# Performance work log

Hardware: AMD Instinct MI355X
Metric: run time of the kernel (lower is better)

The kernel has to match this reference:

```python
import jax, jax.numpy as jnp
import numpy as np

B, S, E = 2, 4096, 512

def setup_inputs() -> dict:
    key = jax.random.key(0)
    kx, kq, kk, kv, ko = jax.random.split(key, 5)
    scale = 1.0 / np.sqrt(E)  # init-style scaling for weights
    return {
        "x": jax.random.normal(kx, (B, S, E), dtype=jnp.float32),
        "Wq": jax.random.normal(kq, (E, E), dtype=jnp.float32) * scale,
        "Wk": jax.random.normal(kk, (E, E), dtype=jnp.float32) * scale,
        "Wv": jax.random.normal(kv, (E, E), dtype=jnp.float32) * scale,
        "Wo": jax.random.normal(ko, (E, E), dtype=jnp.float32) * scale,
        "bo": jnp.zeros((E,), dtype=jnp.float32),
    }

def reference(x, Wq, Wk, Wv, Wo, bo):
    # nn.Linear: y = x @ W.T  (weights stored [out, in])
    q = jnp.einsum("bse,fe->bsf", x, Wq)
    k = jnp.einsum("bse,fe->bsf", x, Wk)
    v = jnp.einsum("bse,fe->bsf", x, Wv)
    inv_scale = 1.0 / jnp.sqrt(jnp.asarray(x.shape[-1], x.dtype))
    scores = jnp.einsum("bqe,bke->bqk", q, k) * inv_scale  # [B,S,S]
    S_len = x.shape[1]
    # torch.triu(ones) keeps j >= i; masked_fill where triu==0 masks j < i
    row = jnp.arange(S_len)[:, None]
    col = jnp.arange(S_len)[None, :]
    keep = col >= row  # [S,S], faithfully anti-causal as in the source
    scores = jnp.where(keep[None, :, :], scores, jnp.asarray(-jnp.inf, scores.dtype))
    attn = jax.nn.softmax(scores, axis=-1)
    # dropout p=0.0 -> identity
    out = jnp.einsum("bqk,bke->bqe", attn, v)
    return jnp.einsum("bse,fe->bsf", out, Wo) + bo
```

## Files before the change

### kernel.cpp

```cpp
#include <hip/hip_runtime.h>
#include <hip/hip_bf16.h>

#define S_LEN 4096
#define E_DIM 512
#define B_DIM 2
#define M_ROWS (B_DIM * S_LEN)

typedef __attribute__((ext_vector_type(8))) short short8;
typedef __attribute__((ext_vector_type(4))) float floatx4;

__device__ __forceinline__ unsigned short f2bf(float f) {
    unsigned u = __float_as_uint(f);
    unsigned r = (u + 0x7fffu + ((u >> 16) & 1u)) >> 16;
    return (unsigned short)r;
}
__device__ __forceinline__ float bf2f(unsigned short u) {
    return __uint_as_float((unsigned)u << 16);
}

__device__ __forceinline__ void async_copy16(unsigned short* lds, const unsigned short* g) {
    auto gp = (const __attribute__((address_space(1))) unsigned int*)g;
    auto lp = (__attribute__((address_space(3))) unsigned int*)lds;
    __builtin_amdgcn_global_load_lds(gp, lp, 16, 0, 0);
}

struct MapArg { unsigned short m[576]; };

__global__ __launch_bounds__(256) void convert_bf16(
    const float* __restrict__ x,  const float* __restrict__ wq,
    const float* __restrict__ wk, const float* __restrict__ wv,
    const float* __restrict__ wo, unsigned short* __restrict__ dstU,
    unsigned short* __restrict__ dstWo)
{
    long i = (long)blockIdx.x * 1024 + (long)threadIdx.x * 4;
    const float* src; long off; unsigned short* dst; long doff;
    if      (i < 4194304) { src = x;  off = i;           dst = dstU;  doff = i; }
    else if (i < 4456448) { src = wq; off = i - 4194304; dst = dstU;  doff = i; }
    else if (i < 4718592) { src = wk; off = i - 4456448; dst = dstU;  doff = i; }
    else if (i < 4980736) { src = wv; off = i - 4718592; dst = dstU;  doff = i; }
    else                  { src = wo; off = i - 4980736; dst = dstWo; doff = i - 4980736; }
    float4 v = *(const float4*)(src + off);
    ushort4 o;
    o.x = f2bf(v.x); o.y = f2bf(v.y); o.z = f2bf(v.z); o.w = f2bf(v.w);
    *(ushort4*)(dst + doff) = o;
}

__device__ __forceinline__ void gemm_core(
    const unsigned short* __restrict__ A, const unsigned short* __restrict__ W,
    void* __restrict__ Cv, const float* __restrict__ bias, int mode,
    int m0, int n0)
{
    __shared__ unsigned short As[128 * 64];
    __shared__ unsigned short Bs[128 * 64];
    const int tid = threadIdx.x;
    const int lane = tid & 63, wave = tid >> 6;
    const int wm = wave >> 1, wn = wave & 1;
    const int q4 = lane >> 4, l16 = lane & 15;
    const int er = l16 & 7;

    floatx4 acc[4][4];
#pragma unroll
    for (int i = 0; i < 4; ++i)
#pragma unroll
        for (int j = 0; j < 4; ++j) acc[i][j] = (floatx4){0.f, 0.f, 0.f, 0.f};

    const int srow = lane >> 3;
    const int scol = ((lane & 7) ^ srow) << 3;

    for (int k0 = 0; k0 < 512; k0 += 64) {
#pragma unroll
        for (int c = 0; c < 4; ++c) {
            const int rbase = c * 32 + wave * 8;
            async_copy16(&As[rbase * 64],
                         A + (size_t)(m0 + rbase + srow) * 512 + k0 + scol);
            async_copy16(&Bs[rbase * 64],
                         W + (size_t)(n0 + rbase + srow) * 512 + k0 + scol);
        }
        __syncthreads();
        short8 af[4][2], bfr[4][2];
        const int c0 = (q4 ^ er) * 8;
#pragma unroll
        for (int i = 0; i < 4; ++i) {
            const int ra = (wm * 64 + i * 16 + l16) * 64;
            const int rb = (wn * 64 + i * 16 + l16) * 64;
            af[i][0]  = *(const short8*)&As[ra + c0];
            af[i][1]  = *(const short8*)&As[ra + (c0 ^ 32)];
            bfr[i][0] = *(const short8*)&Bs[rb + c0];
            bfr[i][1] = *(const short8*)&Bs[rb + (c0 ^ 32)];
        }
#pragma unroll
        for (int h = 0; h < 2; ++h)
#pragma unroll
            for (int i = 0; i < 4; ++i)
#pragma unroll
                for (int j = 0; j < 4; ++j)
                    acc[i][j] = __builtin_amdgcn_mfma_f32_16x16x32_bf16(
                        af[i][h], bfr[j][h], acc[i][j], 0, 0, 0);
        __syncthreads();
    }

    if (mode == 0) {
        unsigned short* C = (unsigned short*)Cv;
#pragma unroll
        for (int i = 0; i < 4; ++i) {
            int rowb = m0 + wm * 64 + i * 16 + q4 * 4;
#pragma unroll
            for (int j = 0; j < 4; ++j) {
                int col = n0 + wn * 64 + j * 16 + l16;
#pragma unroll
                for (int rg = 0; rg < 4; ++rg)
                    C[(size_t)(rowb + rg) * 512 + col] = f2bf(acc[i][j][rg]);
            }
        }
    } else if (mode == 1) {
        unsigned short* C = (unsigned short*)Cv;
#pragma unroll
        for (int i = 0; i < 4; ++i) {
            int grow = m0 + wm * 64 + i * 16 + q4 * 4;
            int b = grow >> 12, s = grow & 4095;
#pragma unroll
            for (int j = 0; j < 4; ++j) {
                int e = n0 + wn * 64 + j * 16 + l16;
                ushort4 pk;
                pk.x = f2bf(acc[i][j][0]); pk.y = f2bf(acc[i][j][1]);
                pk.z = f2bf(acc[i][j][2]); pk.w = f2bf(acc[i][j][3]);
                *(ushort4*)(C + (size_t)b * 512 * 4096 + (size_t)e * 4096 + s) = pk;
            }
        }
    } else {
        float* C = (float*)Cv;
#pragma unroll
        for (int i = 0; i < 4; ++i) {
            int rowb = m0 + wm * 64 + i * 16 + q4 * 4;
#pragma unroll
            for (int j = 0; j < 4; ++j) {
                int col = n0 + wn * 64 + j * 16 + l16;
                float bv = bias[col];
#pragma unroll
                for (int rg = 0; rg < 4; ++rg)
                    C[(size_t)(rowb + rg) * 512 + col] = acc[i][j][rg] + bv;
            }
        }
    }
}

__global__ __launch_bounds__(256) void gemm_qkv(
    const unsigned short* __restrict__ xb,
    const unsigned short* __restrict__ Wqb, const unsigned short* __restrict__ Wkb,
    const unsigned short* __restrict__ Wvb,
    unsigned short* __restrict__ Qb, unsigned short* __restrict__ Kb,
    unsigned short* __restrict__ Vtb)
{
    const int z = blockIdx.z;
    const unsigned short* W = (z == 0) ? Wqb : (z == 1) ? Wkb : Wvb;
    unsigned short* C = (z == 0) ? Qb : (z == 1) ? Kb : Vtb;
    gemm_core(xb, W, C, nullptr, (z == 2) ? 1 : 0, blockIdx.y * 128, blockIdx.x * 128);
}

__global__ __launch_bounds__(256) void gemm_out(
    const unsigned short* __restrict__ AOb, const unsigned short* __restrict__ Wob,
    const float* __restrict__ bo, float* __restrict__ out)
{
    gemm_core(AOb, Wob, out, bo, 2, blockIdx.y * 128, blockIdx.x * 128);
}

__global__ __launch_bounds__(256, 2) void flash_mfma(
    const unsigned short* __restrict__ Qg, const unsigned short* __restrict__ Kg,
    const unsigned short* __restrict__ Vt,
    unsigned short* __restrict__ Oh, float* __restrict__ Lb, MapArg map)
{
    const int enc = map.m[blockIdx.x];
    const int tile = enc & 63, ch = (enc >> 6) & 7, bb = enc >> 9;
    const int i0 = tile * 64;
    const int lo0 = 512 * ch, hi = lo0 + 512;
    const int lo = (i0 > lo0) ? i0 : lo0;
    const int nsteps = (hi - lo) >> 6;

    const int tid = threadIdx.x;
    const int lane = tid & 63, w = tid >> 6;
    const int q4 = lane >> 4, l16 = lane & 15;
    const int e = l16 & 7;
    const float scale = 0.044194173824159216f;
    const float MREF = 4.0f;

    __shared__ unsigned short Qs[64 * 512];
    __shared__ unsigned short Plds[64][72];
    __shared__ float Lred[4][64];

    const size_t rowbase = (size_t)bb * S_LEN;
    const size_t vbase   = (size_t)bb * (size_t)512 * 4096;

#pragma unroll
    for (int rr = 0; rr < 16; ++rr) {
        const int row = w * 16 + rr;
        const unsigned short* src = Qg + (rowbase + i0 + row) * 512
                                    + ((lane ^ (row & 7)) << 3);
        async_copy16(&Qs[row * 512], src);
    }

    floatx4 oacc[4][8];
#pragma unroll
    for (int mg = 0; mg < 4; ++mg)
#pragma unroll
        for (int nc = 0; nc < 8; ++nc) oacc[mg][nc] = (floatx4){0.f, 0.f, 0.f, 0.f};
    float l_acc[4] = {0.f, 0.f, 0.f, 0.f};

    const unsigned short* qb0 = &Qs[l16 * 512 + ((q4 ^ e) << 3)];
    const unsigned short* qb1 = &Qs[l16 * 512 + (((q4 + 4) ^ e) << 3)];
    const unsigned short* kpbase = Kg + (rowbase + 16 * w + l16) * 512 + (q4 << 3);
    const unsigned short* vpbase = Vt + vbase + (size_t)(w * 128 + l16) * 4096 + (q4 << 3);

    __syncthreads();

    for (int t = 0; t < nsteps; ++t) {
        const int j0 = lo + t * 64;

        short8 kf[16];
        const unsigned short* kp = kpbase + (size_t)j0 * 512;
#pragma unroll
        for (int ks = 0; ks < 16; ++ks)
            kf[ks] = *(const short8*)(kp + ks * 32);

        floatx4 sf[4];
#pragma unroll
        for (int mg = 0; mg < 4; ++mg) sf[mg] = (floatx4){0.f, 0.f, 0.f, 0.f};
        __builtin_amdgcn_s_setprio(1);
#pragma unroll
        for (int ks = 0; ks < 16; ++ks) {
            const unsigned short* qb = (ks & 1) ? qb1 : qb0;
#pragma unroll
            for (int mg = 0; mg < 4; ++mg) {
                short8 a = *(const short8*)(qb + mg * 8192 + (ks >> 1) * 64);
                sf[mg] = __builtin_amdgcn_mfma_f32_16x16x32_bf16(kf[ks], a, sf[mg], 0, 0, 0);
            }
        }
        __builtin_amdgcn_s_setprio(0);

        short8 vf[8][2];
#pragma unroll
        for (int nc = 0; nc < 8; ++nc) {
            const unsigned short* vpn = vpbase + (size_t)(nc * 16) * 4096 + j0;
#pragma unroll
            for (int kslot = 0; kslot < 2; ++kslot)
                vf[nc][kslot] = *(const short8*)(vpn + kslot * 32);
        }

        const int kb = j0 + 16 * w + (q4 << 2);
        const bool full = (j0 >= i0 + 64);
        ushort4 pk[4];
#pragma unroll
        for (int mg = 0; mg < 4; ++mg) {
            const int row = i0 + mg * 16 + l16;
            float p0 = __expf(sf[mg][0] * scale - MREF);
            float p1 = __expf(sf[mg][1] * scale - MREF);
            float p2 = __expf(sf[mg][2] * scale - MREF);
            float p3 = __expf(sf[mg][3] * scale - MREF);
            if (!full) {
                p0 = (kb + 0 >= row) ? p0 : 0.f;
                p1 = (kb + 1 >= row) ? p1 : 0.f;
                p2 = (kb + 2 >= row) ? p2 : 0.f;
                p3 = (kb + 3 >= row) ? p3 : 0.f;
            }
            l_acc[mg] += p0 + p1 + p2 + p3;
            pk[mg].x = f2bf(p0); pk[mg].y = f2bf(p1);
            pk[mg].z = f2bf(p2); pk[mg].w = f2bf(p3);
        }

        __syncthreads();

#pragma unroll
        for (int mg = 0; mg < 4; ++mg)
            *(ushort4*)&Plds[mg * 16 + l16][16 * w + (q4 << 2)] = pk[mg];

        __syncthreads();

        __builtin_amdgcn_s_setprio(1);
#pragma unroll
        for (int kslot = 0; kslot < 2; ++kslot) {
#pragma unroll
            for (int mg = 0; mg < 4; ++mg) {
                short8 ap = *(const short8*)&Plds[mg * 16 + l16][kslot * 32 + (q4 << 3)];
#pragma unroll
                for (int nc = 0; nc < 8; ++nc)
                    oacc[mg][nc] = __builtin_amdgcn_mfma_f32_16x16x32_bf16(
                        ap, vf[nc][kslot], oacc[mg][nc], 0, 0, 0);
            }
        }
        __builtin_amdgcn_s_setprio(0);
    }

#pragma unroll
    for (int mg = 0; mg < 4; ++mg) {
        float v = l_acc[mg];
        v += __shfl_xor(v, 16, 64);
        v += __shfl_xor(v, 32, 64);
        if (q4 == 0) Lred[w][mg * 16 + l16] = v;
    }
    __syncthreads();

    const int slot = 8 * ch * (ch + 1) + bb * 8 * (ch + 1) + tile;
    if (tid < 64) {
        float sum = 0.f;
#pragma unroll
        for (int ww = 0; ww < 4; ++ww) sum += Lred[ww][tid];
        Lb[(size_t)slot * 64 + tid] = sum;
    }

    unsigned short* Op = Oh + (size_t)slot * 64 * 512;
#pragma unroll
    for (int mg = 0; mg < 4; ++mg)
#pragma unroll
        for (int nc = 0; nc < 8; ++nc)
#pragma unroll
            for (int rg = 0; rg < 4; ++rg)
                Op[(size_t)(mg * 16 + q4 * 4 + rg) * 512 + w * 128 + nc * 16 + l16]
                    = f2bf(oacc[mg][nc][rg]);
}

__global__ __launch_bounds__(256) void flash_merge(
    const unsigned short* __restrict__ Oh, const float* __restrict__ Lb,
    unsigned short* __restrict__ AO)
{
    const int row = blockIdx.x;
    const int c = threadIdx.x * 2;
    const int bb = row >> 12, i = row & 4095;
    const int t = i >> 6, ri = i & 63;
    const int chmin = i >> 9;
    float lsum = 0.f, v0 = 0.f, v1 = 0.f;
    for (int ch = chmin; ch < 8; ++ch) {
        int slot = 8 * ch * (ch + 1) + bb * 8 * (ch + 1) + t;
        lsum += Lb[(size_t)slot * 64 + ri];
        const unsigned short* p = Oh + (size_t)slot * 64 * 512 + (size_t)ri * 512 + c;
        v0 += bf2f(p[0]);
        v1 += bf2f(p[1]);
    }
    float inv = 1.f / lsum;
    ushort2 o; o.x = f2bf(v0 * inv); o.y = f2bf(v1 * inv);
    *(ushort2*)(AO + (size_t)row * 512 + c) = o;
}

static MapArg build_map() {
    MapArg mp{};
    for (int x = 0; x < 8; ++x) {
        const int bb = x >> 2;
        const int chs[2] = {7 - (x & 3), x & 3};
        int enc[72], st[72], n = 0;
        for (int ci = 0; ci < 2; ++ci) {
            const int ch = chs[ci];
            for (int t = 0; t < 8 * (ch + 1); ++t) {
                int i0 = t * 64, lo0 = 512 * ch, hi = lo0 + 512;
                int lo = (i0 > lo0) ? i0 : lo0;
                enc[n] = t | (ch << 6) | (bb << 9);
                st[n] = (hi - lo) >> 6;
                ++n;
            }
        }
        for (int i = 1; i < n; ++i) {
            int ev = enc[i], sv = st[i], j = i - 1;
            while (j >= 0 && st[j] < sv) { st[j + 1] = st[j]; enc[j + 1] = enc[j]; --j; }
            st[j + 1] = sv; enc[j + 1] = ev;
        }
        for (int j = 0; j < n; ++j) mp.m[x + 8 * j] = (unsigned short)enc[j];
    }
    return mp;
}

extern "C" void kernel_launch(void* const* d_in, const int* in_sizes, int n_in,
                              void* d_out, int out_size, void* d_ws, size_t ws_size,
                              hipStream_t stream) {
    (void)in_sizes; (void)n_in; (void)out_size; (void)ws_size;
    const float* x  = (const float*)d_in[0];
    const float* Wq = (const float*)d_in[1];
    const float* Wk = (const float*)d_in[2];
    const float* Wv = (const float*)d_in[3];
    const float* Wo = (const float*)d_in[4];
    const float* bo = (const float*)d_in[5];
    float* out = (float*)d_out;

    unsigned short* ws  = (unsigned short*)d_ws;
    unsigned short* Wob = ws;
    unsigned short* QAb = ws + 262144;
    unsigned short* Kb  = QAb + 4194304;
    unsigned short* Vtb = Kb + 4194304;
    unsigned short* U   = Vtb + 4194304;
    unsigned short* xb  = U;
    unsigned short* Wqb = U + 4194304;
    unsigned short* Wkb = Wqb + 262144;
    unsigned short* Wvb = Wkb + 262144;
    unsigned short* Ohb = U;
    float* Lbf = (float*)(U + 18874368);

    static const MapArg mp = build_map();

    convert_bf16<<<5120, 256, 0, stream>>>(x, Wq, Wk, Wv, Wo, U, Wob);

    gemm_qkv<<<dim3(4, 64, 3), 256, 0, stream>>>(xb, Wqb, Wkb, Wvb, QAb, Kb, Vtb);

    flash_mfma<<<576, 256, 0, stream>>>(QAb, Kb, Vtb, Ohb, Lbf, mp);

    flash_merge<<<8192, 256, 0, stream>>>(Ohb, Lbf, QAb);

    gemm_out<<<dim3(4, 64), 256, 0, stream>>>(QAb, Wob, bo, out);
}
```

Baseline: 217.0 us.

## Split flash attention block across sixteen waves with double-buffered P tile

Raises the flash kernel from 4 to 16 waves per block. Waves are split into 4 key groups × 4 query-row groups for the QK^T product, and each wave owns a 32-column slice of the output for the PV product. The P tile in LDS is double-buffered, which removes one of the two barriers per step. K fragments are loaded in software-pipelined halves to cut per-thread register pressure and raise latency hiding. The risks are K/V reads now duplicated across waves and the (1024,4) launch bound squeezing the register budget hard enough to cause spills, while the ~83KB LDS per block likely limits the CU to one resident block.

```diff
diff --git a/kernel.cpp b/kernel.cpp
--- a/kernel.cpp
+++ b/kernel.cpp
@@ -164,7 +164,7 @@
     gemm_core(AOb, Wob, out, bo, 2, blockIdx.y * 128, blockIdx.x * 128);
 }
 
-__global__ __launch_bounds__(256, 2) void flash_mfma(
+__global__ __launch_bounds__(1024, 4) void flash_mfma(
     const unsigned short* __restrict__ Qg, const unsigned short* __restrict__ Kg,
     const unsigned short* __restrict__ Vt,
     unsigned short* __restrict__ Oh, float* __restrict__ Lb, MapArg map)
@@ -178,131 +178,126 @@
 
     const int tid = threadIdx.x;
     const int lane = tid & 63, w = tid >> 6;
+    const int kg = w & 3, qrg = w >> 2;
     const int q4 = lane >> 4, l16 = lane & 15;
     const int e = l16 & 7;
     const float scale = 0.044194173824159216f;
     const float MREF = 4.0f;
 
     __shared__ unsigned short Qs[64 * 512];
-    __shared__ unsigned short Plds[64][72];
+    __shared__ unsigned short Plds[2][64][72];
     __shared__ float Lred[4][64];
 
     const size_t rowbase = (size_t)bb * S_LEN;
     const size_t vbase   = (size_t)bb * (size_t)512 * 4096;
 
 #pragma unroll
-    for (int rr = 0; rr < 16; ++rr) {
-        const int row = w * 16 + rr;
+    for (int rr = 0; rr < 4; ++rr) {
+        const int row = w * 4 + rr;
         const unsigned short* src = Qg + (rowbase + i0 + row) * 512
                                     + ((lane ^ (row & 7)) << 3);
         async_copy16(&Qs[row * 512], src);
     }
 
-    floatx4 oacc[4][8];
-#pragma unroll
-    for (int mg = 0; mg < 4; ++mg)
-#pragma unroll
-        for (int nc = 0; nc < 8; ++nc) oacc[mg][nc] = (floatx4){0.f, 0.f, 0.f, 0.f};
-    float l_acc[4] = {0.f, 0.f, 0.f, 0.f};
-
-    const unsigned short* qb0 = &Qs[l16 * 512 + ((q4 ^ e) << 3)];
-    const unsigned short* qb1 = &Qs[l16 * 512 + (((q4 + 4) ^ e) << 3)];
-    const unsigned short* kpbase = Kg + (rowbase + 16 * w + l16) * 512 + (q4 << 3);
-    const unsigned short* vpbase = Vt + vbase + (size_t)(w * 128 + l16) * 4096 + (q4 << 3);
+    floatx4 oacc[4][2];
+#pragma unroll
+    for (int mg = 0; mg < 4; ++mg) {
+        oacc[mg][0] = (floatx4){0.f, 0.f, 0.f, 0.f};
+        oacc[mg][1] = (floatx4){0.f, 0.f, 0.f, 0.f};
+    }
+    float l_acc = 0.f;
+
+    const unsigned short* qbase = &Qs[(16 * qrg + l16) * 512];
+    const unsigned short* kpbase = Kg + (rowbase + 16 * kg + l16) * 512 + (q4 << 3);
+    const unsigned short* vpbase = Vt + vbase + (size_t)(32 * w + l16) * 4096 + (q4 << 3);
 
     __syncthreads();
+
+#define QREAD(ks) (*(const short8*)(qbase + (((((ks) << 2) | q4) ^ e) << 3)))
 
     for (int t = 0; t < nsteps; ++t) {
         const int j0 = lo + t * 64;
-
-        short8 kf[16];
+        const int buf = t & 1;
         const unsigned short* kp = kpbase + (size_t)j0 * 512;
-#pragma unroll
-        for (int ks = 0; ks < 16; ++ks)
-            kf[ks] = *(const short8*)(kp + ks * 32);
-
-        floatx4 sf[4];
-#pragma unroll
-        for (int mg = 0; mg < 4; ++mg) sf[mg] = (floatx4){0.f, 0.f, 0.f, 0.f};
+
+        floatx4 sf = (floatx4){0.f, 0.f, 0.f, 0.f};
+        short8 k0[4], k1[4];
+#pragma unroll
+        for (int kk = 0; kk < 4; ++kk) k0[kk] = *(const short8*)(kp + kk * 32);
+#pragma unroll
+        for (int kk = 0; kk < 4; ++kk) k1[kk] = *(const short8*)(kp + 128 + kk * 32);
         __builtin_amdgcn_s_setprio(1);
 #pragma unroll
-        for (int ks = 0; ks < 16; ++ks) {
-            const unsigned short* qb = (ks & 1) ? qb1 : qb0;
-#pragma unroll
-            for (int mg = 0; mg < 4; ++mg) {
-                short8 a = *(const short8*)(qb + mg * 8192 + (ks >> 1) * 64);
-                sf[mg] = __builtin_amdgcn_mfma_f32_16x16x32_bf16(kf[ks], a, sf[mg], 0, 0, 0);
-            }
-        }
+        for (int kk = 0; kk < 4; ++kk)
+            sf = __builtin_amdgcn_mfma_f32_16x16x32_bf16(k0[kk], QREAD(kk), sf, 0, 0, 0);
+#pragma unroll
+        for (int kk = 0; kk < 4; ++kk) k0[kk] = *(const short8*)(kp + 256 + kk * 32);
+#pragma unroll
+        for (int kk = 0; kk < 4; ++kk)
+            sf = __builtin_amdgcn_mfma_f32_16x16x32_bf16(k1[kk], QREAD(4 + kk), sf, 0, 0, 0);
+#pragma unroll
+        for (int kk = 0; kk < 4; ++kk) k1[kk] = *(const short8*)(kp + 384 + kk * 32);
+#pragma unroll
+        for (int kk = 0; kk < 4; ++kk)
+            sf = __builtin_amdgcn_mfma_f32_16x16x32_bf16(k0[kk], QREAD(8 + kk), sf, 0, 0, 0);
+#pragma unroll
+        for (int kk = 0; kk < 4; ++kk)
+            sf = __builtin_amdgcn_mfma_f32_16x16x32_bf16(k1[kk], QREAD(12 + kk), sf, 0, 0, 0);
         __builtin_amdgcn_s_setprio(0);
 
-        short8 vf[8][2];
-#pragma unroll
-        for (int nc = 0; nc < 8; ++nc) {
-            const unsigned short* vpn = vpbase + (size_t)(nc * 16) * 4096 + j0;
-#pragma unroll
-            for (int kslot = 0; kslot < 2; ++kslot)
-                vf[nc][kslot] = *(const short8*)(vpn + kslot * 32);
-        }
-
-        const int kb = j0 + 16 * w + (q4 << 2);
-        const bool full = (j0 >= i0 + 64);
-        ushort4 pk[4];
-#pragma unroll
-        for (int mg = 0; mg < 4; ++mg) {
-            const int row = i0 + mg * 16 + l16;
-            float p0 = __expf(sf[mg][0] * scale - MREF);
-            float p1 = __expf(sf[mg][1] * scale - MREF);
-            float p2 = __expf(sf[mg][2] * scale - MREF);
-            float p3 = __expf(sf[mg][3] * scale - MREF);
-            if (!full) {
+        short8 vfa0 = *(const short8*)(vpbase + j0);
+        short8 vfa1 = *(const short8*)(vpbase + j0 + 32);
+        short8 vfb0 = *(const short8*)(vpbase + (size_t)16 * 4096 + j0);
+        short8 vfb1 = *(const short8*)(vpbase + (size_t)16 * 4096 + j0 + 32);
+
+        {
+            const int kb = j0 + 16 * kg + (q4 << 2);
+            const int row = i0 + 16 * qrg + l16;
+            float p0 = __expf(sf[0] * scale - MREF);
+            float p1 = __expf(sf[1] * scale - MREF);
+            float p2 = __expf(sf[2] * scale - MREF);
+            float p3 = __expf(sf[3] * scale - MREF);
+            if (j0 < i0 + 64) {
                 p0 = (kb + 0 >= row) ? p0 : 0.f;
                 p1 = (kb + 1 >= row) ? p1 : 0.f;
                 p2 = (kb + 2 >= row) ? p2 : 0.f;
                 p3 = (kb + 3 >= row) ? p3 : 0.f;
             }
-            l_acc[mg] += p0 + p1 + p2 + p3;
-            pk[mg].x = f2bf(p0); pk[mg].y = f2bf(p1);
-            pk[mg].z = f2bf(p2); pk[mg].w = f2bf(p3);
+            l_acc += p0 + p1 + p2 + p3;
+            ushort4 pk;
+            pk.x = f2bf(p0); pk.y = f2bf(p1); pk.z = f2bf(p2); pk.w = f2bf(p3);
+            *(ushort4*)&Plds[buf][16 * qrg + l16][16 * kg + (q4 << 2)] = pk;
         }
 
         __syncthreads();
 
-#pragma unroll
-        for (int mg = 0; mg < 4; ++mg)
-            *(ushort4*)&Plds[mg * 16 + l16][16 * w + (q4 << 2)] = pk[mg];
-
-        __syncthreads();
-
         __builtin_amdgcn_s_setprio(1);
 #pragma unroll
-        for (int kslot = 0; kslot < 2; ++kslot) {
+        for (int ks2 = 0; ks2 < 2; ++ks2) {
 #pragma unroll
             for (int mg = 0; mg < 4; ++mg) {
-                short8 ap = *(const short8*)&Plds[mg * 16 + l16][kslot * 32 + (q4 << 3)];
-#pragma unroll
-                for (int nc = 0; nc < 8; ++nc)
-                    oacc[mg][nc] = __builtin_amdgcn_mfma_f32_16x16x32_bf16(
-                        ap, vf[nc][kslot], oacc[mg][nc], 0, 0, 0);
+                short8 ap = *(const short8*)&Plds[buf][mg * 16 + l16][ks2 * 32 + (q4 << 3)];
+                oacc[mg][0] = __builtin_amdgcn_mfma_f32_16x16x32_bf16(
+                    ap, ks2 ? vfa1 : vfa0, oacc[mg][0], 0, 0, 0);
+                oacc[mg][1] = __builtin_amdgcn_mfma_f32_16x16x32_bf16(
+                    ap, ks2 ? vfb1 : vfb0, oacc[mg][1], 0, 0, 0);
             }
         }
         __builtin_amdgcn_s_setprio(0);
     }
-
-#pragma unroll
-    for (int mg = 0; mg < 4; ++mg) {
-        float v = l_acc[mg];
+#undef QREAD
+
+    {
+        float v = l_acc;
         v += __shfl_xor(v, 16, 64);
         v += __shfl_xor(v, 32, 64);
-        if (q4 == 0) Lred[w][mg * 16 + l16] = v;
+        if (q4 == 0) Lred[kg][16 * qrg + l16] = v;
     }
     __syncthreads();
 
     const int slot = 8 * ch * (ch + 1) + bb * 8 * (ch + 1) + tile;
     if (tid < 64) {
-        float sum = 0.f;
-#pragma unroll
-        for (int ww = 0; ww < 4; ++ww) sum += Lred[ww][tid];
+        float sum = Lred[0][tid] + Lred[1][tid] + Lred[2][tid] + Lred[3][tid];
         Lb[(size_t)slot * 64 + tid] = sum;
     }
 
@@ -310,11 +305,11 @@
 #pragma unroll
     for (int mg = 0; mg < 4; ++mg)
 #pragma unroll
-        for (int nc = 0; nc < 8; ++nc)
-#pragma unroll
-            for (int rg = 0; rg < 4; ++rg)
-                Op[(size_t)(mg * 16 + q4 * 4 + rg) * 512 + w * 128 + nc * 16 + l16]
-                    = f2bf(oacc[mg][nc][rg]);
+        for (int nc = 0; nc < 2; ++nc)
+#pragma unroll
+            for (int rg2 = 0; rg2 < 4; ++rg2)
+                Op[(size_t)(mg * 16 + q4 * 4 + rg2) * 512 + 32 * w + nc * 16 + l16]
+                    = f2bf(oacc[mg][nc][rg2]);
 }
 
 __global__ __launch_bounds__(256) void flash_merge(
@@ -396,7 +391,7 @@
 
     gemm_qkv<<<dim3(4, 64, 3), 256, 0, stream>>>(xb, Wqb, Wkb, Wvb, QAb, Kb, Vtb);
 
-    flash_mfma<<<576, 256, 0, stream>>>(QAb, Kb, Vtb, Ohb, Lbf, mp);
+    flash_mfma<<<576, 1024, 0, stream>>>(QAb, Kb, Vtb, Ohb, Lbf, mp);
 
     flash_merge<<<8192, 256, 0, stream>>>(Ohb, Lbf, QAb);
 
```

Measured after the change: 311.0 us. 43.3% more time.
